# Kernel tuning notes

Measured on AMD Instinct MI355X. Metric: run time of the kernel, lower is better.

## Reference

```python
import jax, jax.numpy as jnp
from jax import lax
import numpy as np

EPS = 1e-5

def _sign(v):
    # sign with sign(0) = +1, as in standard binarized nets
    return jnp.where(v >= 0, 1.0, -1.0).astype(v.dtype)

def binarize(v):
    # forward: sign(v); backward: straight-through with hardtanh clipping
    ht = jnp.clip(v, -1.0, 1.0)
    return ht + lax.stop_gradient(_sign(v) - ht)

def conv2d(x, w, b, pad):
    y = lax.conv_general_dilated(
        x, w, window_strides=(1, 1),
        padding=[(pad, pad), (pad, pad)],
        dimension_numbers=('NCHW', 'OIHW', 'NCHW'))
    return y + b[None, :, None, None]

def batchnorm(x, gamma, beta):
    # training-mode BN over (N, H, W) per channel
    m = jnp.mean(x, axis=(0, 2, 3), keepdims=True)
    v = jnp.var(x, axis=(0, 2, 3), keepdims=True)
    xn = (x - m) * lax.rsqrt(v + EPS)
    return xn * gamma[None, :, None, None] + beta[None, :, None, None]

def maxpool2(x):
    return lax.reduce_window(x, -jnp.inf, lax.max,
                             (1, 1, 2, 2), (1, 1, 2, 2), 'VALID')

def setup_inputs() -> dict:
    key = jax.random.key(0)
    ks = jax.random.split(key, 8)
    B = 8192
    return {
        'x': jax.random.normal(ks[0], (B, 1, 28, 28), jnp.float32),
        'conv1_w': jax.random.normal(ks[1], (16, 1, 5, 5), jnp.float32) * 0.2,
        'conv1_b': jax.random.normal(ks[2], (16,), jnp.float32) * 0.1,
        'bn1_g': jnp.ones((16,), jnp.float32),
        'bn1_b': jnp.zeros((16,), jnp.float32),
        'conv2_w': jax.random.normal(ks[3], (32, 16, 5, 5), jnp.float32) * 0.2,
        'conv2_b': jax.random.normal(ks[4], (32,), jnp.float32) * 0.1,
        'bn2_g': jnp.ones((32,), jnp.float32),
        'bn2_b': jnp.zeros((32,), jnp.float32),
        'fc_w': jax.random.normal(ks[5], (10, 7 * 7 * 32), jnp.float32) * 0.2,
        'fc_b': jax.random.normal(ks[6], (10,), jnp.float32) * 0.1,
    }

def reference(x, conv1_w, conv1_b, bn1_g, bn1_b,
              conv2_w, conv2_b, bn2_g, bn2_b, fc_w, fc_b):
    # block 1: binary conv -> BN -> maxpool -> binary tanh
    out = conv2d(x, binarize(conv1_w), conv1_b, pad=2)      # [B,16,28,28]
    out = batchnorm(out, bn1_g, bn1_b)
    out = maxpool2(out)                                      # [B,16,14,14]
    out = binarize(out)                                      # BinaryTanh
    # block 2
    out = conv2d(out, binarize(conv2_w), conv2_b, pad=2)     # [B,32,14,14]
    out = batchnorm(out, bn2_g, bn2_b)
    out = maxpool2(out)                                      # [B,32,7,7]
    out = binarize(out)
    # binary linear classifier
    out = out.reshape(out.shape[0], -1)                      # [B,1568]
    return out @ binarize(fc_w).T + fc_b                     # [B,10]
```

## Files before the change

### kernel.cpp

```cpp
#include <hip/hip_runtime.h>
#include <stdint.h>

#define BATCH 8192
#define H1 28
#define W1 28
#define C1 16
#define P1 14
#define C2 32
#define P2 7

#define NPIX1  (BATCH*H1*W1)
#define NPOOL1 (BATCH*P1*P1)
#define NPOOL2 (BATCH*P2*P2)

#define QD_BLOCKS 3136
#define A1S_BLOCKS 6272
#define C2F_BLOCKS 6272

typedef float f32x2 __attribute__((ext_vector_type(2)));

__global__ __launch_bounds__(256) void k_prep(const float* __restrict__ w1,
                                              const float* __restrict__ w2,
                                              const float* __restrict__ fcw,
                                              const float* __restrict__ g1,
                                              const float* __restrict__ g2,
                                              unsigned* __restrict__ w1s,
                                              unsigned short* __restrict__ w2b,
                                              unsigned* __restrict__ w2p,
                                              unsigned short* __restrict__ w2k,
                                              unsigned* __restrict__ fcp,
                                              unsigned* __restrict__ selb) {
    for (int c = threadIdx.x; c < 16; c += blockDim.x) {
        unsigned sb = 0;
        for (int i = 0; i < 25; ++i)
            if (w1[c*25 + i] < 0.f) sb |= 1u << i;
        w1s[c] = sb;
    }
    for (int i = threadIdx.x; i < 800; i += blockDim.x) {
        int co = i / 25, kk = i % 25;
        unsigned m = 0;
        for (int ci = 0; ci < 16; ++ci)
            if (w2[co*400 + ci*25 + kk] >= 0.f) m |= 1u << ci;
        w2b[i] = (unsigned short)m;
    }
    for (int i = threadIdx.x; i < 32*13; i += blockDim.x) {
        int co = i / 13, j = i % 13;
        int k1, k2;
        if (j < 10)      { k1 = (j/2)*5 + (j&1)*2; k2 = k1 + 1; }
        else if (j == 10){ k1 = 4;  k2 = 9;  }
        else if (j == 11){ k1 = 14; k2 = 19; }
        else             { k1 = 24; k2 = -1; }
        unsigned lo = 0, hi = 0;
        for (int ci = 0; ci < 16; ++ci) {
            if (w2[co*400 + ci*25 + k1] >= 0.f) lo |= 1u << ci;
            if (k2 >= 0 && w2[co*400 + ci*25 + k2] >= 0.f) hi |= 1u << ci;
        }
        w2p[i] = lo | (hi << 16);
    }
    for (int i = threadIdx.x; i < 3920; i += blockDim.x) {
        int j = i / 392, g = i % 392;
        unsigned v = 0;
        for (int by = 0; by < 4; ++by) {
            int k = g*4 + by;
            unsigned char s = (fcw[j*1568 + k] >= 0.f) ? 0x01 : 0xFF;
            v |= ((unsigned)s) << (8*by);
        }
        fcp[i] = v;
    }
    if (threadIdx.x == 0) {
        unsigned s1 = 0, s2 = 0;
        for (int c = 0; c < 16; ++c) if (g1[c] < 0.f) s1 |= 1u << c;
        for (int c = 0; c < 32; ++c) if (g2[c] < 0.f) s2 |= 1u << c;
        selb[0] = s1; selb[1] = s2;
    }
    __syncthreads();
    {
        const int lo5[5] = {2,1,0,0,0};
        const int hi5[5] = {4,4,4,3,2};
        for (int i = threadIdx.x; i < 800; i += blockDim.x) {
            int cls = i >> 5, co = i & 31;
            int rc = cls / 5, cc = cls % 5;
            int rlo = lo5[rc], rhi = hi5[rc], clo = lo5[cc], chi = hi5[cc];
            int C = 0;
            for (int ky = 0; ky < 5; ++ky)
                for (int kx = 0; kx < 5; ++kx)
                    if (ky < rlo || ky > rhi || kx < clo || kx > chi)
                        C += __popc((unsigned)w2b[co*25 + ky*5 + kx]);
            int nv = (rhi - rlo + 1) * (chi - clo + 1);
            w2k[i] = (unsigned short)(16*nv + 2*C);
        }
    }
}

__global__ __launch_bounds__(256) void k_conv1_quad(const float* __restrict__ x,
                                                    const unsigned* __restrict__ w1s,
                                                    const float* __restrict__ b1,
                                                    const unsigned* __restrict__ selb,
                                                    float* __restrict__ ext1,
                                                    double* __restrict__ partial1) {
    const int wave = threadIdx.x >> 6, lane = threadIdx.x & 63;
    const int half = wave & 1;
    const int pg   = wave >> 1;
    const int c0   = half << 3;
    unsigned selbs = __builtin_amdgcn_readfirstlane(selb[0]);

    float bv[8];
#pragma unroll
    for (int cl = 0; cl < 8; ++cl) bv[cl] = b1[c0 + cl];

    const int qq = blockIdx.x*128 + pg*64 + lane;
    const int b  = qq / 49;
    const int rr = qq % 49;
    const int qy = rr / 7, qx = rr % 7;
    const float* xb = x + (size_t)b * (H1*W1);

    const int ix0 = 4*qx - 2;
    const bool cL = (qx == 0), cR = (qx == 6);
    const int o0 = cL ? 0 : ix0;
    const int o3 = cR ? 24 : ix0 + 6;

    float xd[64];
#pragma unroll
    for (int dy = 0; dy < 8; ++dy) {
        int iy = 4*qy + dy - 2;
        bool rv = (iy >= 0) && (iy < H1);
        const float* rp = xb + (rv ? iy : 0)*W1;
        f32x2 p0 = *(const f32x2*)(rp + o0);
        f32x2 p1 = *(const f32x2*)(rp + ix0 + 2);
        f32x2 p2 = *(const f32x2*)(rp + ix0 + 4);
        f32x2 p3 = *(const f32x2*)(rp + o3);
        bool vL = rv && !cL, vR = rv && !cR;
        xd[dy*8+0] = vL ? p0.x : 0.f;
        xd[dy*8+1] = vL ? p0.y : 0.f;
        xd[dy*8+2] = rv ? p1.x : 0.f;
        xd[dy*8+3] = rv ? p1.y : 0.f;
        xd[dy*8+4] = rv ? p2.x : 0.f;
        xd[dy*8+5] = rv ? p2.y : 0.f;
        xd[dy*8+6] = vR ? p3.x : 0.f;
        xd[dy*8+7] = vR ? p3.y : 0.f;
    }

    double s[8], q[8];
#pragma unroll
    for (int i = 0; i < 8; ++i) { s[i] = 0.0; q[i] = 0.0; }

#pragma unroll
    for (int cl = 0; cl < 8; ++cl) {
        unsigned sb = __builtin_amdgcn_readfirstlane(w1s[c0 + cl]);
        f32x2 y00={0.f,0.f}, y01={0.f,0.f}, y10={0.f,0.f}, y11={0.f,0.f};
        f32x2 y20={0.f,0.f}, y21={0.f,0.f}, y30={0.f,0.f}, y31={0.f,0.f};
#pragma unroll
        for (int ky = 0; ky < 5; ++ky) {
#pragma unroll
            for (int kx = 0; kx < 5; ++kx) {
                float m = __uint_as_float(0x3F800000u ^
                            (((sb >> (ky*5 + kx)) & 1u) << 31));
                f32x2 mm = {m, m};
                f32x2 a0 = { xd[(0+ky)*8 + kx    ], xd[(0+ky)*8 + kx + 1] };
                f32x2 a1 = { xd[(0+ky)*8 + kx + 2], xd[(0+ky)*8 + kx + 3] };
                f32x2 b0 = { xd[(1+ky)*8 + kx    ], xd[(1+ky)*8 + kx + 1] };
                f32x2 b1v= { xd[(1+ky)*8 + kx + 2], xd[(1+ky)*8 + kx + 3] };
                f32x2 c0v= { xd[(2+ky)*8 + kx    ], xd[(2+ky)*8 + kx + 1] };
                f32x2 c1 = { xd[(2+ky)*8 + kx + 2], xd[(2+ky)*8 + kx + 3] };
                f32x2 d0 = { xd[(3+ky)*8 + kx    ], xd[(3+ky)*8 + kx + 1] };
                f32x2 d1 = { xd[(3+ky)*8 + kx + 2], xd[(3+ky)*8 + kx + 3] };
                y00 = a0*mm + y00;  y01 = a1*mm + y01;
                y10 = b0*mm + y10;  y11 = b1v*mm + y11;
                y20 = c0v*mm + y20; y21 = c1*mm + y21;
                y30 = d0*mm + y30;  y31 = d1*mm + y31;
            }
        }
        float bb = bv[cl];
        f32x2 bb2 = {bb, bb};
        y00 += bb2; y01 += bb2; y10 += bb2; y11 += bb2;
        y20 += bb2; y21 += bb2; y30 += bb2; y31 += bb2;

        int c = c0 + cl;
        int sel = (selbs >> c) & 1;
        float e00 = sel ? fminf(fminf(y00.x,y00.y), fminf(y10.x,y10.y))
                        : fmaxf(fmaxf(y00.x,y00.y), fmaxf(y10.x,y10.y));
        float e01 = sel ? fminf(fminf(y01.x,y01.y), fminf(y11.x,y11.y))
                        : fmaxf(fmaxf(y01.x,y01.y), fmaxf(y11.x,y11.y));
        float e10 = sel ? fminf(fminf(y20.x,y20.y), fminf(y30.x,y30.y))
                        : fmaxf(fmaxf(y20.x,y20.y), fmaxf(y30.x,y30.y));
        float e11 = sel ? fminf(fminf(y21.x,y21.y), fminf(y31.x,y31.y))
                        : fmaxf(fmaxf(y21.x,y21.y), fmaxf(y31.x,y31.y));
        size_t base = (size_t)c*NPOOL1 + (size_t)b*(P1*P1) + (2*qy)*P1 + 2*qx;
        f32x2 ev0 = {e00, e01};
        f32x2 ev1 = {e10, e11};
        *(f32x2*)(ext1 + base)      = ev0;
        *(f32x2*)(ext1 + base + P1) = ev1;

        f32x2 sp = ((y00 + y01) + (y10 + y11)) + ((y20 + y21) + (y30 + y31));
        f32x2 qp = y00*y00;
        qp = y01*y01 + qp; qp = y10*y10 + qp; qp = y11*y11 + qp;
        qp = y20*y20 + qp; qp = y21*y21 + qp; qp = y30*y30 + qp;
        qp = y31*y31 + qp;
        s[cl] += (double)(sp.x + sp.y);
        q[cl] += (double)(qp.x + qp.y);
    }

    __shared__ double lsum[4][8], lsq[4][8];
#pragma unroll
    for (int cl = 0; cl < 8; ++cl) {
        double ss = s[cl], qq2 = q[cl];
#pragma unroll
        for (int off = 32; off; off >>= 1) {
            ss  += __shfl_down(ss, off);
            qq2 += __shfl_down(qq2, off);
        }
        if (lane == 0) { lsum[wave][cl] = ss; lsq[wave][cl] = qq2; }
    }
    __syncthreads();
    if (threadIdx.x < 16) {
        int c = threadIdx.x;
        int w0 = (c < 8) ? 0 : 1, cl = c & 7;
        partial1[(size_t)blockIdx.x*32 + c] = lsum[w0][cl] + lsum[w0+2][cl];
    } else if (threadIdx.x < 32) {
        int c = threadIdx.x - 16;
        int w0 = (c < 8) ? 0 : 1, cl = c & 7;
        partial1[(size_t)blockIdx.x*32 + 16 + c] = lsq[w0][cl] + lsq[w0+2][cl];
    }
}

__global__ __launch_bounds__(256) void k_finalize1(const double* __restrict__ part,
                                                   int nblk,
                                                   const float* __restrict__ g,
                                                   const float* __restrict__ be,
                                                   double* __restrict__ thr,
                                                   int* __restrict__ mode) {
    int c = blockIdx.x;
    double s = 0, q = 0;
    for (int i = threadIdx.x; i < nblk; i += 256) {
        s += part[(size_t)i*32 + c];
        q += part[(size_t)i*32 + 16 + c];
    }
    __shared__ double ls[256], lq[256];
    ls[threadIdx.x] = s; lq[threadIdx.x] = q;
    __syncthreads();
    for (int st = 128; st > 0; st >>= 1) {
        if (threadIdx.x < st) {
            ls[threadIdx.x] += ls[threadIdx.x + st];
            lq[threadIdx.x] += lq[threadIdx.x + st];
        }
        __syncthreads();
    }
    if (threadIdx.x == 0) {
        double N = (double)NPIX1;
        double m = ls[0] / N;
        double var = lq[0] / N - m*m;
        double gamma = (double)g[c], beta = (double)be[c];
        double sc = gamma / sqrt(var + 1e-5);
        int md; double tt = 0.0;
        if (sc > 0)      { md = 0; tt = m - beta / sc; }
        else if (sc < 0) { md = 1; tt = m - beta / sc; }
        else             { md = (beta >= 0) ? 2 : 3; }
        thr[c] = tt; mode[c] = md;
    }
}

__global__ __launch_bounds__(256) void k_sign1(const float* __restrict__ ext1,
                                               const double* __restrict__ thr,
                                               const int* __restrict__ mode,
                                               unsigned short* __restrict__ a1b) {
    int t = blockIdx.x*256 + threadIdx.x;
    unsigned bits = 0;
#pragma unroll
    for (int c = 0; c < 16; ++c) {
        float v = ext1[(size_t)c*NPOOL1 + t];
        int md = mode[c]; double tt = thr[c];
        bool plus = (md == 0) ? ((double)v >= tt)
                  : (md == 1) ? ((double)v <= tt)
                  : (md == 2);
        bits |= (plus ? 1u : 0u) << c;
    }
    a1b[t] = (unsigned short)bits;
}

__global__ __launch_bounds__(256) void k_conv2_fused(const unsigned short* __restrict__ a1b,
                                                     const unsigned* __restrict__ w2p,
                                                     const unsigned short* __restrict__ w2k,
                                                     const unsigned* __restrict__ selb,
                                                     short* __restrict__ ext2,
                                                     int* __restrict__ partial2) {
    __shared__ unsigned short raw[3*18*18];
    __shared__ unsigned sw[32*13];
    __shared__ unsigned short kt[25*32];
    __shared__ int lsum[4][32], lsq[4][32];

    const int B0 = blockIdx.x * 64;
    const int i0 = B0 / 49;
    const int ilast = (B0 + 63) / 49;
    const int icnt = ilast - i0 + 1;

    for (int i = threadIdx.x; i < 416; i += 256) sw[i] = w2p[i];
    for (int i = threadIdx.x; i < 800; i += 256) kt[i] = w2k[i];
    {
        unsigned* rz = (unsigned*)raw;
        int n32 = icnt * 162;
        for (int i = threadIdx.x; i < n32; i += 256) rz[i] = 0u;
    }
    __syncthreads();
    {
        int n = icnt * 196;
        for (int e = threadIdx.x; e < n; e += 256) {
            int img = e / 196, lin = e % 196;
            unsigned short v = a1b[(size_t)(i0 + img)*196 + lin];
            int py = lin / 14, px = lin % 14;
            raw[(img*18 + py + 2)*18 + px + 2] = v;
        }
    }
    __syncthreads();

    const int quarter = threadIdx.x & 3;
    const int c0 = quarter << 3;
    const int t = B0 + (threadIdx.x >> 2);
    const int img = t / 49 - i0;
    const int r = t % 49;
    const int qy = r / 7, qx = r % 7;
    const unsigned selbs = __builtin_amdgcn_readfirstlane(selb[1]);

    unsigned am[36];
#pragma unroll
    for (int wy = 0; wy < 6; ++wy)
#pragma unroll
        for (int wx = 0; wx < 6; ++wx)
            am[wy*6 + wx] = (unsigned)raw[(img*18 + 2*qy + wy)*18 + 2*qx + wx];

    int s[8], q[8], mx[8], mn[8];
#pragma unroll
    for (int i = 0; i < 8; ++i) { s[i]=0; q[i]=0; mx[i]=-1000000; mn[i]=1000000; }

#pragma unroll
    for (int sp = 0; sp < 4; ++sp) {
        const int sy = sp >> 1, sx = sp & 1;
        const int oy = 2*qy + sy, ox = 2*qx + sx;
        const int rcls = (oy < 2) ? oy : ((oy > 11) ? oy - 9 : 2);
        const int ccls = (ox < 2) ? ox : ((ox > 11) ? ox - 9 : 2);
        const int kbase = (rcls*5 + ccls) * 32 + c0;

        unsigned ap[13];
#pragma unroll
        for (int ky = 0; ky < 5; ++ky) {
            ap[ky*2+0] = am[(sy+ky)*6 + sx+0] | (am[(sy+ky)*6 + sx+1] << 16);
            ap[ky*2+1] = am[(sy+ky)*6 + sx+2] | (am[(sy+ky)*6 + sx+3] << 16);
        }
        ap[10] = am[(sy+0)*6 + sx+4] | (am[(sy+1)*6 + sx+4] << 16);
        ap[11] = am[(sy+2)*6 + sx+4] | (am[(sy+3)*6 + sx+4] << 16);
        ap[12] = am[(sy+4)*6 + sx+4];

#pragma unroll
        for (int cl = 0; cl < 8; ++cl) {
            const unsigned* wr = sw + (c0 + cl)*13;
            int p = 0;
#pragma unroll
            for (int j = 0; j < 13; ++j)
                p += __popc(ap[j] ^ wr[j]);
            int y = (int)kt[kbase + cl] - 2*p;
            s[cl] += y; q[cl] += y*y;
            mx[cl] = (y > mx[cl]) ? y : mx[cl];
            mn[cl] = (y < mn[cl]) ? y : mn[cl];
        }
    }

#pragma unroll
    for (int cl = 0; cl < 8; ++cl) {
        int co = c0 + cl;
        int sel = (selbs >> co) & 1;
        ext2[(size_t)co*NPOOL2 + t] = (short)(sel ? mn[cl] : mx[cl]);
    }

    int wave = threadIdx.x >> 6, lane = threadIdx.x & 63;
#pragma unroll
    for (int cl = 0; cl < 8; ++cl) {
        int ss = s[cl], qq = q[cl];
#pragma unroll
        for (int off = 32; off >= 4; off >>= 1) {
            ss += __shfl_down(ss, off);
            qq += __shfl_down(qq, off);
        }
        if (lane < 4) {
            lsum[wave][lane*8 + cl] = ss;
            lsq[wave][lane*8 + cl]  = qq;
        }
    }
    __syncthreads();
    if (threadIdx.x < 32) {
        int co = threadIdx.x;
        partial2[(size_t)blockIdx.x*64 + co] =
            lsum[0][co] + lsum[1][co] + lsum[2][co] + lsum[3][co];
    } else if (threadIdx.x < 64) {
        int co = threadIdx.x - 32;
        partial2[(size_t)blockIdx.x*64 + 32 + co] =
            lsq[0][co] + lsq[1][co] + lsq[2][co] + lsq[3][co];
    }
}

__global__ __launch_bounds__(256) void k_finalize2i(const int* __restrict__ part,
                                                    int nblk,
                                                    const float* __restrict__ b2,
                                                    const float* __restrict__ g,
                                                    const float* __restrict__ be,
                                                    double* __restrict__ thr,
                                                    int* __restrict__ mode) {
    int c = blockIdx.x;
    long long s = 0, q = 0;
    for (int i = threadIdx.x; i < nblk; i += 256) {
        s += (long long)part[(size_t)i*64 + c];
        q += (long long)part[(size_t)i*64 + 32 + c];
    }
    __shared__ long long ls[256], lq[256];
    ls[threadIdx.x] = s; lq[threadIdx.x] = q;
    __syncthreads();
    for (int st = 128; st > 0; st >>= 1) {
        if (threadIdx.x < st) {
            ls[threadIdx.x] += ls[threadIdx.x + st];
            lq[threadIdx.x] += lq[threadIdx.x + st];
        }
        __syncthreads();
    }
    if (threadIdx.x == 0) {
        double N = (double)(BATCH * P1 * P1);
        double my = (double)ls[0] / N;
        double var = (double)lq[0] / N - my*my;
        double m = my + (double)b2[c];
        double gamma = (double)g[c], beta = (double)be[c];
        double sc = gamma / sqrt(var + 1e-5);
        int md; double tt = 0.0;
        if (sc > 0)      { md = 0; tt = m - beta / sc; }
        else if (sc < 0) { md = 1; tt = m - beta / sc; }
        else             { md = (beta >= 0) ? 2 : 3; }
        thr[c] = tt; mode[c] = md;
    }
}

__global__ __launch_bounds__(256) void k_sign2(const short* __restrict__ ext2,
                                               const float* __restrict__ b2,
                                               const double* __restrict__ thr,
                                               const int* __restrict__ mode,
                                               char* __restrict__ a2) {
    int t = blockIdx.x*256 + threadIdx.x;
    int b = t / (P2*P2);
    int r = t % (P2*P2);
#pragma unroll 1
    for (int co = 0; co < 32; ++co) {
        short v = ext2[(size_t)co*NPOOL2 + t];
        float yf = (float)v + b2[co];
        int md = mode[co]; double tt = thr[co];
        bool plus = (md == 0) ? ((double)yf >= tt)
                  : (md == 1) ? ((double)yf <= tt)
                  : (md == 2);
        a2[(size_t)b*1568 + co*49 + r] = plus ? (char)1 : (char)-1;
    }
}

__global__ __launch_bounds__(256) void k_fc(const char* __restrict__ a2,
                                            const unsigned* __restrict__ fcp,
                                            const float* __restrict__ fcb,
                                            float* __restrict__ out) {
    int t = blockIdx.x*256 + threadIdx.x;
    int b = t / 10, j = t % 10;
    const unsigned* ar = (const unsigned*)(a2 + (size_t)b*1568);
    const unsigned* wr = fcp + j*392;
    int p = 0;
    for (int g = 0; g < 392; ++g)
        p += __popc((ar[g] ^ wr[g]) & 0x02020202u);
    out[t] = (float)(1568 - 2*p) + fcb[j];
}

extern "C" void kernel_launch(void* const* d_in, const int* in_sizes, int n_in,
                              void* d_out, int out_size, void* d_ws, size_t ws_size,
                              hipStream_t stream) {
    const float* x    = (const float*)d_in[0];
    const float* w1   = (const float*)d_in[1];
    const float* b1   = (const float*)d_in[2];
    const float* bn1g = (const float*)d_in[3];
    const float* bn1b = (const float*)d_in[4];
    const float* w2   = (const float*)d_in[5];
    const float* b2   = (const float*)d_in[6];
    const float* bn2g = (const float*)d_in[7];
    const float* bn2b = (const float*)d_in[8];
    const float* fcw  = (const float*)d_in[9];
    const float* fcb  = (const float*)d_in[10];
    float* out = (float*)d_out;

    char* ws = (char*)d_ws;
    size_t cur = 0;
    auto alloc = [&](size_t sz) {
        size_t o = cur;
        cur += (sz + 255) & ~(size_t)255;
        return o;
    };
    unsigned*       w1s      = (unsigned*)(ws + alloc(16 * 4));
    unsigned short* w2b      = (unsigned short*)(ws + alloc(800 * 2));
    unsigned*       w2p      = (unsigned*)(ws + alloc(416 * 4));
    unsigned short* w2k      = (unsigned short*)(ws + alloc(800 * 2));
    unsigned*       fcp      = (unsigned*)(ws + alloc(3920 * 4));
    unsigned*       selb     = (unsigned*)(ws + alloc(2 * 4));
    double*         thr1     = (double*)(ws + alloc(16 * 8));
    int*            mode1    = (int*)(ws + alloc(16 * 4));
    double*         thr2     = (double*)(ws + alloc(32 * 8));
    int*            mode2    = (int*)(ws + alloc(32 * 4));
    double*         partial1 = (double*)(ws + alloc((size_t)QD_BLOCKS * 32 * 8));
    int*            partial2 = (int*)(ws + alloc((size_t)C2F_BLOCKS * 64 * 4));
    unsigned short* a1b      = (unsigned short*)(ws + alloc((size_t)NPOOL1 * 2));
    char*           a2       = (char*)(ws + alloc((size_t)BATCH * 1568));
    size_t extoff = alloc((size_t)C1 * NPOOL1 * 4);
    float* ext1 = (float*)(ws + extoff);
    short* ext2 = (short*)(ws + extoff);

    k_prep<<<1, 256, 0, stream>>>(w1, w2, fcw, bn1g, bn2g,
                                  w1s, w2b, w2p, w2k, fcp, selb);
    k_conv1_quad<<<QD_BLOCKS, 256, 0, stream>>>(x, w1s, b1, selb, ext1, partial1);
    k_finalize1<<<16, 256, 0, stream>>>(partial1, QD_BLOCKS, bn1g, bn1b, thr1, mode1);
    k_sign1<<<A1S_BLOCKS, 256, 0, stream>>>(ext1, thr1, mode1, a1b);
    k_conv2_fused<<<C2F_BLOCKS, 256, 0, stream>>>(a1b, w2p, w2k, selb, ext2, partial2);
    k_finalize2i<<<32, 256, 0, stream>>>(partial2, C2F_BLOCKS, b2, bn2g, bn2b, thr2, mode2);
    k_sign2<<<NPOOL2/256, 256, 0, stream>>>(ext2, b2, thr2, mode2, a2);
    k_fc<<<320, 256, 0, stream>>>(a2, fcp, fcb, out);
}
```

Baseline: 263.4 us.

## Fuse sign2 with FC via shared memory and parallelize weight prep

Merges the second binarization kernel and the FC popcount kernel into one kernel that writes the sign bytes for 16 images to shared memory and runs the classifier from there, removing the a2 global round-trip and one launch. Weight prep is split across 13 blocks instead of running serially in one block, with w2b kept in shared memory. conv1 reduces its per-channel BN statistics inside the channel loop instead of holding 16 double accumulators, which lowers register pressure. The fused kernel launches only 512 blocks using about 25KB of LDS each, so occupancy and the FC inner loop may limit it.

```diff
diff --git a/kernel.cpp b/kernel.cpp
--- a/kernel.cpp
+++ b/kernel.cpp
@@ -16,6 +16,8 @@
 #define QD_BLOCKS 3136
 #define A1S_BLOCKS 6272
 #define C2F_BLOCKS 6272
+#define SF_IMGS   16
+#define SF_BLOCKS 512
 
 typedef float f32x2 __attribute__((ext_vector_type(2)));
 
@@ -25,59 +27,52 @@
                                               const float* __restrict__ g1,
                                               const float* __restrict__ g2,
                                               unsigned* __restrict__ w1s,
-                                              unsigned short* __restrict__ w2b,
                                               unsigned* __restrict__ w2p,
                                               unsigned short* __restrict__ w2k,
                                               unsigned* __restrict__ fcp,
                                               unsigned* __restrict__ selb) {
-    for (int c = threadIdx.x; c < 16; c += blockDim.x) {
-        unsigned sb = 0;
-        for (int i = 0; i < 25; ++i)
-            if (w1[c*25 + i] < 0.f) sb |= 1u << i;
-        w1s[c] = sb;
-    }
-    for (int i = threadIdx.x; i < 800; i += blockDim.x) {
-        int co = i / 25, kk = i % 25;
-        unsigned m = 0;
-        for (int ci = 0; ci < 16; ++ci)
-            if (w2[co*400 + ci*25 + kk] >= 0.f) m |= 1u << ci;
-        w2b[i] = (unsigned short)m;
-    }
-    for (int i = threadIdx.x; i < 32*13; i += blockDim.x) {
-        int co = i / 13, j = i % 13;
-        int k1, k2;
-        if (j < 10)      { k1 = (j/2)*5 + (j&1)*2; k2 = k1 + 1; }
-        else if (j == 10){ k1 = 4;  k2 = 9;  }
-        else if (j == 11){ k1 = 14; k2 = 19; }
-        else             { k1 = 24; k2 = -1; }
-        unsigned lo = 0, hi = 0;
-        for (int ci = 0; ci < 16; ++ci) {
-            if (w2[co*400 + ci*25 + k1] >= 0.f) lo |= 1u << ci;
-            if (k2 >= 0 && w2[co*400 + ci*25 + k2] >= 0.f) hi |= 1u << ci;
-        }
-        w2p[i] = lo | (hi << 16);
-    }
-    for (int i = threadIdx.x; i < 3920; i += blockDim.x) {
-        int j = i / 392, g = i % 392;
-        unsigned v = 0;
-        for (int by = 0; by < 4; ++by) {
-            int k = g*4 + by;
-            unsigned char s = (fcw[j*1568 + k] >= 0.f) ? 0x01 : 0xFF;
-            v |= ((unsigned)s) << (8*by);
-        }
-        fcp[i] = v;
-    }
-    if (threadIdx.x == 0) {
-        unsigned s1 = 0, s2 = 0;
-        for (int c = 0; c < 16; ++c) if (g1[c] < 0.f) s1 |= 1u << c;
-        for (int c = 0; c < 32; ++c) if (g2[c] < 0.f) s2 |= 1u << c;
-        selb[0] = s1; selb[1] = s2;
-    }
-    __syncthreads();
-    {
+    const int blk = blockIdx.x;
+    if (blk == 0) {
+        for (int c = threadIdx.x; c < 16; c += 256) {
+            unsigned sb = 0;
+            for (int i = 0; i < 25; ++i)
+                if (w1[c*25 + i] < 0.f) sb |= 1u << i;
+            w1s[c] = sb;
+        }
+        if (threadIdx.x == 0) {
+            unsigned s1 = 0, s2 = 0;
+            for (int c = 0; c < 16; ++c) if (g1[c] < 0.f) s1 |= 1u << c;
+            for (int c = 0; c < 32; ++c) if (g2[c] < 0.f) s2 |= 1u << c;
+            selb[0] = s1; selb[1] = s2;
+        }
+    } else if (blk == 1) {
+        for (int i = threadIdx.x; i < 32*13; i += 256) {
+            int co = i / 13, j = i % 13;
+            int k1, k2;
+            if (j < 10)      { k1 = (j/2)*5 + (j&1)*2; k2 = k1 + 1; }
+            else if (j == 10){ k1 = 4;  k2 = 9;  }
+            else if (j == 11){ k1 = 14; k2 = 19; }
+            else             { k1 = 24; k2 = -1; }
+            unsigned lo = 0, hi = 0;
+            for (int ci = 0; ci < 16; ++ci) {
+                if (w2[co*400 + ci*25 + k1] >= 0.f) lo |= 1u << ci;
+                if (k2 >= 0 && w2[co*400 + ci*25 + k2] >= 0.f) hi |= 1u << ci;
+            }
+            w2p[i] = lo | (hi << 16);
+        }
+    } else if (blk == 2) {
+        __shared__ unsigned short sw2b[800];
+        for (int i = threadIdx.x; i < 800; i += 256) {
+            int co = i / 25, kk = i % 25;
+            unsigned m = 0;
+            for (int ci = 0; ci < 16; ++ci)
+                if (w2[co*400 + ci*25 + kk] >= 0.f) m |= 1u << ci;
+            sw2b[i] = (unsigned short)m;
+        }
+        __syncthreads();
         const int lo5[5] = {2,1,0,0,0};
         const int hi5[5] = {4,4,4,3,2};
-        for (int i = threadIdx.x; i < 800; i += blockDim.x) {
+        for (int i = threadIdx.x; i < 800; i += 256) {
             int cls = i >> 5, co = i & 31;
             int rc = cls / 5, cc = cls % 5;
             int rlo = lo5[rc], rhi = hi5[rc], clo = lo5[cc], chi = hi5[cc];
@@ -85,9 +80,22 @@
             for (int ky = 0; ky < 5; ++ky)
                 for (int kx = 0; kx < 5; ++kx)
                     if (ky < rlo || ky > rhi || kx < clo || kx > chi)
-                        C += __popc((unsigned)w2b[co*25 + ky*5 + kx]);
+                        C += __popc((unsigned)sw2b[co*25 + ky*5 + kx]);
             int nv = (rhi - rlo + 1) * (chi - clo + 1);
             w2k[i] = (unsigned short)(16*nv + 2*C);
+        }
+    } else {
+        int i0 = (blk - 3) * 392;
+        for (int ii = threadIdx.x; ii < 392; ii += 256) {
+            int i = i0 + ii;
+            int j = i / 392, g = i % 392;
+            unsigned v = 0;
+            for (int by = 0; by < 4; ++by) {
+                int k = g*4 + by;
+                unsigned char s = (fcw[j*1568 + k] >= 0.f) ? 0x01 : 0xFF;
+                v |= ((unsigned)s) << (8*by);
+            }
+            fcp[i] = v;
         }
     }
 }
@@ -140,9 +148,7 @@
         xd[dy*8+7] = vR ? p3.y : 0.f;
     }
 
-    double s[8], q[8];
-#pragma unroll
-    for (int i = 0; i < 8; ++i) { s[i] = 0.0; q[i] = 0.0; }
+    __shared__ double lsum[4][8], lsq[4][8];
 
 #pragma unroll
     for (int cl = 0; cl < 8; ++cl) {
@@ -196,21 +202,16 @@
         qp = y01*y01 + qp; qp = y10*y10 + qp; qp = y11*y11 + qp;
         qp = y20*y20 + qp; qp = y21*y21 + qp; qp = y30*y30 + qp;
         qp = y31*y31 + qp;
-        s[cl] += (double)(sp.x + sp.y);
-        q[cl] += (double)(qp.x + qp.y);
-    }
-
-    __shared__ double lsum[4][8], lsq[4][8];
-#pragma unroll
-    for (int cl = 0; cl < 8; ++cl) {
-        double ss = s[cl], qq2 = q[cl];
+        double ssd = (double)(sp.x + sp.y);
+        double qqd = (double)(qp.x + qp.y);
 #pragma unroll
         for (int off = 32; off; off >>= 1) {
-            ss  += __shfl_down(ss, off);
-            qq2 += __shfl_down(qq2, off);
-        }
-        if (lane == 0) { lsum[wave][cl] = ss; lsq[wave][cl] = qq2; }
-    }
+            ssd += __shfl_down(ssd, off);
+            qqd += __shfl_down(qqd, off);
+        }
+        if (lane == 0) { lsum[wave][cl] = ssd; lsq[wave][cl] = qqd; }
+    }
+
     __syncthreads();
     if (threadIdx.x < 16) {
         int c = threadIdx.x;
@@ -434,38 +435,50 @@
     }
 }
 
-__global__ __launch_bounds__(256) void k_sign2(const short* __restrict__ ext2,
-                                               const float* __restrict__ b2,
-                                               const double* __restrict__ thr,
-                                               const int* __restrict__ mode,
-                                               char* __restrict__ a2) {
-    int t = blockIdx.x*256 + threadIdx.x;
-    int b = t / (P2*P2);
-    int r = t % (P2*P2);
+__global__ __launch_bounds__(256) void k_sign2fc(const short* __restrict__ ext2,
+                                                 const float* __restrict__ b2,
+                                                 const double* __restrict__ thr,
+                                                 const int* __restrict__ mode,
+                                                 const unsigned* __restrict__ fcp,
+                                                 const float* __restrict__ fcb,
+                                                 float* __restrict__ out) {
+    __shared__ char a2l[SF_IMGS*1568];
+    __shared__ float sb[32];
+    __shared__ double sthr[32];
+    __shared__ int smd[32];
+    if (threadIdx.x < 32) {
+        sb[threadIdx.x]   = b2[threadIdx.x];
+        sthr[threadIdx.x] = thr[threadIdx.x];
+        smd[threadIdx.x]  = mode[threadIdx.x];
+    }
+    __syncthreads();
+
+    const int b0 = blockIdx.x * SF_IMGS;
+    for (int e = threadIdx.x; e < SF_IMGS*49; e += 256) {
+        int il = e / 49, r = e % 49;
+        int t = (b0 + il)*49 + r;
 #pragma unroll 1
-    for (int co = 0; co < 32; ++co) {
-        short v = ext2[(size_t)co*NPOOL2 + t];
-        float yf = (float)v + b2[co];
-        int md = mode[co]; double tt = thr[co];
-        bool plus = (md == 0) ? ((double)yf >= tt)
-                  : (md == 1) ? ((double)yf <= tt)
-                  : (md == 2);
-        a2[(size_t)b*1568 + co*49 + r] = plus ? (char)1 : (char)-1;
-    }
-}
-
-__global__ __launch_bounds__(256) void k_fc(const char* __restrict__ a2,
-                                            const unsigned* __restrict__ fcp,
-                                            const float* __restrict__ fcb,
-                                            float* __restrict__ out) {
-    int t = blockIdx.x*256 + threadIdx.x;
-    int b = t / 10, j = t % 10;
-    const unsigned* ar = (const unsigned*)(a2 + (size_t)b*1568);
-    const unsigned* wr = fcp + j*392;
-    int p = 0;
-    for (int g = 0; g < 392; ++g)
-        p += __popc((ar[g] ^ wr[g]) & 0x02020202u);
-    out[t] = (float)(1568 - 2*p) + fcb[j];
+        for (int co = 0; co < 32; ++co) {
+            short v = ext2[(size_t)co*NPOOL2 + t];
+            float yf = (float)v + sb[co];
+            int md = smd[co]; double tt = sthr[co];
+            bool plus = (md == 0) ? ((double)yf >= tt)
+                      : (md == 1) ? ((double)yf <= tt)
+                      : (md == 2);
+            a2l[il*1568 + co*49 + r] = plus ? (char)1 : (char)-1;
+        }
+    }
+    __syncthreads();
+
+    for (int o = threadIdx.x; o < SF_IMGS*10; o += 256) {
+        int il = o / 10, j = o % 10;
+        const unsigned* ar = (const unsigned*)(a2l + il*1568);
+        const unsigned* wr = fcp + j*392;
+        int p = 0;
+        for (int g = 0; g < 392; ++g)
+            p += __popc((ar[g] ^ wr[g]) & 0x02020202u);
+        out[(b0 + il)*10 + j] = (float)(1568 - 2*p) + fcb[j];
+    }
 }
 
 extern "C" void kernel_launch(void* const* d_in, const int* in_sizes, int n_in,
@@ -492,7 +505,6 @@
         return o;
     };
     unsigned*       w1s      = (unsigned*)(ws + alloc(16 * 4));
-    unsigned short* w2b      = (unsigned short*)(ws + alloc(800 * 2));
     unsigned*       w2p      = (unsigned*)(ws + alloc(416 * 4));
     unsigned short* w2k      = (unsigned short*)(ws + alloc(800 * 2));
     unsigned*       fcp      = (unsigned*)(ws + alloc(3920 * 4));
@@ -504,18 +516,16 @@
     double*         partial1 = (double*)(ws + alloc((size_t)QD_BLOCKS * 32 * 8));
     int*            partial2 = (int*)(ws + alloc((size_t)C2F_BLOCKS * 64 * 4));
     unsigned short* a1b      = (unsigned short*)(ws + alloc((size_t)NPOOL1 * 2));
-    char*           a2       = (char*)(ws + alloc((size_t)BATCH * 1568));
     size_t extoff = alloc((size_t)C1 * NPOOL1 * 4);
     float* ext1 = (float*)(ws + extoff);
     short* ext2 = (short*)(ws + extoff);
 
-    k_prep<<<1, 256, 0, stream>>>(w1, w2, fcw, bn1g, bn2g,
-                                  w1s, w2b, w2p, w2k, fcp, selb);
+    k_prep<<<13, 256, 0, stream>>>(w1, w2, fcw, bn1g, bn2g,
+                                   w1s, w2p, w2k, fcp, selb);
     k_conv1_quad<<<QD_BLOCKS, 256, 0, stream>>>(x, w1s, b1, selb, ext1, partial1);
     k_finalize1<<<16, 256, 0, stream>>>(partial1, QD_BLOCKS, bn1g, bn1b, thr1, mode1);
     k_sign1<<<A1S_BLOCKS, 256, 0, stream>>>(ext1, thr1, mode1, a1b);
     k_conv2_fused<<<C2F_BLOCKS, 256, 0, stream>>>(a1b, w2p, w2k, selb, ext2, partial2);
     k_finalize2i<<<32, 256, 0, stream>>>(partial2, C2F_BLOCKS, b2, bn2g, bn2b, thr2, mode2);
-    k_sign2<<<NPOOL2/256, 256, 0, stream>>>(ext2, b2, thr2, mode2, a2);
-    k_fc<<<320, 256, 0, stream>>>(a2, fcp, fcb, out);
-}
+    k_sign2fc<<<SF_BLOCKS, 256, 0, stream>>>(ext2, b2, thr2, mode2, fcp, fcb, out);
+}
```

Result: faster. 258.1 us (-2.0%).
